# Optimization experiments

Measured on AMD Instinct MI355X. Metric: run time of the kernel, lower is better.

Reference implementation:

```python
import jax, jax.numpy as jnp
import numpy as np

RADIUS = 50.0
EPS = 1e-8


def setup_inputs() -> dict:
    key = jax.random.key(0)
    k1, k2, k3, k4, k5 = jax.random.split(key, 5)
    N, E, H = 16384, 524288, 256
    x = jax.random.normal(k1, (N, H), dtype=jnp.float32)
    edge_index = jax.random.randint(k2, (2, E), 0, N, dtype=jnp.int32)
    spatial_coords = jax.random.uniform(k3, (N, 2), dtype=jnp.float32) * 1000.0
    w1 = jax.random.normal(k4, (3, H // 2), dtype=jnp.float32) * 0.02
    b1 = jnp.zeros((H // 2,), dtype=jnp.float32)
    w2 = jax.random.normal(k5, (H // 2, H), dtype=jnp.float32) * 0.02
    b2 = jnp.zeros((H,), dtype=jnp.float32)
    return {"x": x, "edge_index": edge_index, "spatial_coords": spatial_coords,
            "w1": w1, "b1": b1, "w2": w2, "b2": b2}


def reference(x, edge_index, spatial_coords, w1, b1, w2, b2):
    N = x.shape[0]
    row, col = edge_index[0], edge_index[1]

    # degree via scatter-add (segment_sum)
    ones = jnp.ones(row.shape, dtype=x.dtype)
    degree = jax.ops.segment_sum(ones, row, num_segments=N)  # [N]

    # spatial density: count neighbors within RADIUS (full pairwise, vectorized)
    sq = jnp.sum(spatial_coords * spatial_coords, axis=-1)  # [N]
    d2 = sq[:, None] + sq[None, :] - 2.0 * (spatial_coords @ spatial_coords.T)  # [N,N] squared dists
    in_radius = (d2 <= RADIUS * RADIUS).astype(x.dtype)
    density = jnp.sum(in_radius, axis=1) - 1.0  # exclude self
    density = density / (jnp.max(density) + EPS)

    # local feature variance: || x - mean(neighbor features) ||
    nbr_sum = jax.ops.segment_sum(x[col], row, num_segments=N)  # [N,H]
    cnt = jnp.clip(degree, 1.0)[:, None]
    nbr_mean = nbr_sum / cnt
    fvar = jnp.linalg.norm(x - nbr_mean, axis=-1)  # [N]
    fvar = fvar / (jnp.max(fvar) + EPS)

    feats = jnp.stack([degree / (jnp.max(degree) + EPS), density, fvar], axis=-1)  # [N,3]
    h = jax.nn.relu(feats @ w1 + b1)
    return h @ w2 + b2  # [N, hidden_dim]
```

## Files before the change

kernel.cpp:

```cpp
#include <hip/hip_runtime.h>
#include <math.h>

#define R2 2500.0f
#define EPSF 1e-8f

constexpr int H   = 256;
constexpr int HH  = 128;
constexpr int NB  = 8;
constexpr int BSH = 11;
constexpr int RPW = 4;

__global__ void k_degree(const int* __restrict__ row, const int* __restrict__ col,
                         int* __restrict__ deg4, int E) {
    int e = blockIdx.x * blockDim.x + threadIdx.x;
    if (e < E) atomicAdd(&deg4[row[e] * NB + (col[e] >> BSH)], 1);
}

__global__ void __launch_bounds__(256) k_bsum(const int* __restrict__ deg4,
                                              int* __restrict__ bsum) {
    int t = threadIdx.x;
    int4 v = ((const int4*)deg4)[blockIdx.x * 256 + t];
    int sum = v.x + v.y + v.z + v.w;
#pragma unroll
    for (int off = 32; off > 0; off >>= 1) sum += __shfl_xor(sum, off, 64);
    __shared__ int sw[4];
    if ((t & 63) == 0) sw[t >> 6] = sum;
    __syncthreads();
    if (t == 0) bsum[blockIdx.x] = sw[0] + sw[1] + sw[2] + sw[3];
}

__global__ void k_bscan(const int* __restrict__ bsum, int* __restrict__ boff) {
    __shared__ int s[128];
    int t = threadIdx.x;
    s[t] = bsum[t];
    __syncthreads();
    for (int off = 1; off < 128; off <<= 1) {
        int v = s[t];
        int add = (t >= off) ? s[t - off] : 0;
        __syncthreads();
        s[t] = v + add;
        __syncthreads();
    }
    boff[t] = (t > 0) ? s[t - 1] : 0;
}

__global__ void __launch_bounds__(256) k_scat(const int* __restrict__ deg4,
                                              const int* __restrict__ boff,
                                              int* __restrict__ rp4,
                                              int* __restrict__ cur4, int M) {
    int t = threadIdx.x, blk = blockIdx.x;
    int lane = t & 63, w = t >> 6;
    int4 v = ((const int4*)deg4)[blk * 256 + t];
    int tsum = v.x + v.y + v.z + v.w;
    int incl = tsum;
#pragma unroll
    for (int off = 1; off < 64; off <<= 1) {
        int n = __shfl_up(incl, off, 64);
        if (lane >= off) incl += n;
    }
    __shared__ int wsum[4];
    if (lane == 63) wsum[w] = incl;
    __syncthreads();
    int woff = 0;
#pragma unroll
    for (int k = 0; k < 4; k++) woff += (k < w) ? wsum[k] : 0;
    int excl = boff[blk] + woff + (incl - tsum);
    int4 r;
    r.x = excl;
    r.y = excl + v.x;
    r.z = excl + v.x + v.y;
    r.w = excl + v.x + v.y + v.z;
    ((int4*)rp4)[blk * 256 + t]  = r;
    ((int4*)cur4)[blk * 256 + t] = r;
    if (blk == gridDim.x - 1 && t == 255) rp4[M] = excl + tsum;
}

__global__ void k_fill(const int* __restrict__ row, const int* __restrict__ col,
                       int* __restrict__ cur4, int* __restrict__ cols, int E) {
    int e = blockIdx.x * blockDim.x + threadIdx.x;
    if (e < E) {
        int r = row[e], c = col[e];
        int p = atomicAdd(&cur4[r * NB + (c >> BSH)], 1);
        cols[p] = c;
    }
}

__global__ void k_cellcnt(const float* __restrict__ coords, int* __restrict__ cellcnt, int N) {
    int t = blockIdx.x * 256 + threadIdx.x;
    float2 c = ((const float2*)coords)[t];
    int cx = (int)(c.x * 0.02f); if (cx > 19) cx = 19;
    int cy = (int)(c.y * 0.02f); if (cy > 19) cy = 19;
    atomicAdd(&cellcnt[cy * 20 + cx], 1);
}

__global__ void k_cellscan(const int* __restrict__ cellcnt, int* __restrict__ cellstart,
                           int* __restrict__ cellcur) {
    __shared__ int s[512];
    int t = threadIdx.x;
    s[t] = (t < 400) ? cellcnt[t] : 0;
    __syncthreads();
    for (int off = 1; off < 512; off <<= 1) {
        int v = s[t];
        int add = (t >= off) ? s[t - off] : 0;
        __syncthreads();
        s[t] = v + add;
        __syncthreads();
    }
    if (t < 400) {
        int excl = (t > 0) ? s[t - 1] : 0;
        cellstart[t] = excl;
        cellcur[t]   = excl;
    }
    if (t == 400) cellstart[400] = s[399];
}

__global__ void k_cellfill(const float* __restrict__ coords, int* __restrict__ cellcur,
                           float4* __restrict__ pts, int N) {
    int t = blockIdx.x * 256 + threadIdx.x;
    float2 c = ((const float2*)coords)[t];
    int cx = (int)(c.x * 0.02f); if (cx > 19) cx = 19;
    int cy = (int)(c.y * 0.02f); if (cy > 19) cy = 19;
    int p = atomicAdd(&cellcur[cy * 20 + cx], 1);
    pts[p] = make_float4(c.x, c.y, c.x * c.x + c.y * c.y, __int_as_float(t));
}

__global__ void __launch_bounds__(256) k_dgrid(
    const float4* __restrict__ pts, const int* __restrict__ cellstart,
    int* __restrict__ dens, int N) {
    int wave = threadIdx.x >> 6;
    int lane = threadIdx.x & 63;
    int t = blockIdx.x * 4 + wave;
    float4 p = pts[t];
    int cx = (int)(p.x * 0.02f); if (cx > 19) cx = 19;
    int cy = (int)(p.y * 0.02f); if (cy > 19) cy = 19;
    int x0 = cx - 2; if (x0 < 0) x0 = 0;
    int x1 = cx + 2; if (x1 > 19) x1 = 19;
    int y0 = cy - 2; if (y0 < 0) y0 = 0;
    int y1 = cy + 2; if (y1 > 19) y1 = 19;
    int cnt = 0;
    for (int yy = y0; yy <= y1; yy++) {
        int rowb = yy * 20;
        int s = cellstart[rowb + x0];
        int e = cellstart[rowb + x1 + 1];
        for (int q = s + lane; q < e; q += 64) {
            float4 pq = pts[q];
            float dot = p.x * pq.x + p.y * pq.y;
            float d2 = (p.z + pq.z) - 2.0f * dot;
            cnt += (d2 <= R2) ? 1 : 0;
        }
    }
#pragma unroll
    for (int off = 32; off > 0; off >>= 1) cnt += __shfl_xor(cnt, off, 64);
    if (lane == 0) dens[__float_as_int(p.w)] = cnt;
}

__global__ void __launch_bounds__(256) k_fvar(
    const float* __restrict__ x, const int* __restrict__ rp4,
    const int* __restrict__ cols, float* __restrict__ fvar, int N) {
    __shared__ float4 lds[4][8][64];
    int wave = threadIdx.x >> 6;
    int lane = threadIdx.x & 63;
    int i0 = (blockIdx.x * 4 + wave) * RPW;
    const float4* xb = (const float4*)x;
    float4 acc[RPW];
#pragma unroll
    for (int r = 0; r < RPW; r++) acc[r] = make_float4(0.f, 0.f, 0.f, 0.f);

    for (int b = 0; b < NB; b++) {
#pragma unroll
        for (int r = 0; r < RPW; r++) {
            int s = rp4[(i0 + r) * NB + b];
            int e = rp4[(i0 + r) * NB + b + 1];
            for (int p0 = s; p0 < e; p0 += 64) {
                int m = e - p0; if (m > 64) m = 64;
                int idx = cols[p0 + (lane < m ? lane : m - 1)];
                for (int j = 0; j < m; j += 8) {
                    int nb2 = m - j; if (nb2 > 8) nb2 = 8;
#pragma unroll
                    for (int k = 0; k < 8; k++) {
                        if (k < nb2) {
                            int c = __shfl(idx, j + k, 64);
                            const float4* gp = xb + (size_t)c * 64 + lane;
                            __builtin_amdgcn_global_load_lds(
                                (const __attribute__((address_space(1))) void*)gp,
                                (__attribute__((address_space(3))) void*)(&lds[wave][k][0]),
                                16, 0, 0);
                        }
                    }
                    __builtin_amdgcn_s_waitcnt(0);
#pragma unroll
                    for (int k = 0; k < 8; k++) {
                        if (k < nb2) {
                            float4 v = lds[wave][k][lane];
                            acc[r].x += v.x; acc[r].y += v.y;
                            acc[r].z += v.z; acc[r].w += v.w;
                        }
                    }
                }
            }
        }
    }

#pragma unroll
    for (int r = 0; r < RPW; r++) {
        int i = i0 + r;
        float cnt = fmaxf((float)(rp4[(i + 1) * NB] - rp4[i * NB]), 1.0f);
        float4 xi = xb[(size_t)i * 64 + lane];
        float dx = xi.x - acc[r].x / cnt;
        float dy = xi.y - acc[r].y / cnt;
        float dz = xi.z - acc[r].z / cnt;
        float dw = xi.w - acc[r].w / cnt;
        float ss = dx * dx + dy * dy + dz * dz + dw * dw;
#pragma unroll
        for (int off = 32; off > 0; off >>= 1) ss += __shfl_xor(ss, off, 64);
        if (lane == 0) fvar[i] = sqrtf(ss);
    }
}

__global__ void __launch_bounds__(256) k_scal(
    const int* __restrict__ rp4, const int* __restrict__ dens,
    const float* __restrict__ fvar, int* __restrict__ scal, int N) {
    __shared__ int sd[4], sn[4];
    __shared__ float sf[4];
    int t = threadIdx.x;
    int g = blockIdx.x * 256 + t;
    int stride = 256 * gridDim.x;
    int md = 0, mn = 0;
    float mf = 0.f;
    for (int i = g; i < N; i += stride) {
        md = max(md, rp4[(i + 1) * NB] - rp4[i * NB]);
        mn = max(mn, dens[i]);
        mf = fmaxf(mf, fvar[i]);
    }
#pragma unroll
    for (int off = 32; off > 0; off >>= 1) {
        md = max(md, __shfl_xor(md, off, 64));
        mn = max(mn, __shfl_xor(mn, off, 64));
        mf = fmaxf(mf, __shfl_xor(mf, off, 64));
    }
    int w = t >> 6, l = t & 63;
    if (l == 0) { sd[w] = md; sn[w] = mn; sf[w] = mf; }
    __syncthreads();
    if (t == 0) {
#pragma unroll
        for (int k = 1; k < 4; k++) {
            md = max(md, sd[k]);
            mn = max(mn, sn[k]);
            mf = fmaxf(mf, sf[k]);
        }
        atomicMax(&scal[0], md);
        atomicMax(&scal[1], mn);
        atomicMax(&scal[2], __float_as_int(mf));
    }
}

__global__ void __launch_bounds__(256) k_mlp(
    const float* __restrict__ w1, const float* __restrict__ b1,
    const float* __restrict__ w2, const float* __restrict__ b2,
    const int* __restrict__ rp4, const int* __restrict__ dens,
    const float* __restrict__ fvar, const int* __restrict__ scal,
    float* __restrict__ out, int N) {
    __shared__ float sh_h[HH];
    int j = threadIdx.x;
    float wv[HH];
#pragma unroll
    for (int l = 0; l < HH; l++) wv[l] = w2[l * H + j];
    float bj = b2[j];
    float maxdeg  = (float)scal[0] + EPSF;
    float maxdens = (float)(scal[1] - 1) + EPSF;
    float maxfv   = __int_as_float(scal[2]) + EPSF;
    float w1a = 0.f, w1b = 0.f, w1c = 0.f, b1j = 0.f;
    if (j < HH) { w1a = w1[j]; w1b = w1[HH + j]; w1c = w1[2 * HH + j]; b1j = b1[j]; }
    for (int i = blockIdx.x; i < N; i += gridDim.x) {
        float f0 = (float)(rp4[(i + 1) * NB] - rp4[i * NB]) / maxdeg;
        float f1 = (float)(dens[i] - 1) / maxdens;
        float f2 = fvar[i] / maxfv;
        if (j < HH) {
            float h = f0 * w1a + f1 * w1b + f2 * w1c + b1j;
            sh_h[j] = fmaxf(h, 0.0f);
        }
        __syncthreads();
        float acc = bj;
#pragma unroll
        for (int l = 0; l < HH; l++) acc = fmaf(sh_h[l], wv[l], acc);
        out[(size_t)i * H + j] = acc;
        __syncthreads();
    }
}

extern "C" void kernel_launch(void* const* d_in, const int* in_sizes, int n_in,
                              void* d_out, int out_size, void* d_ws, size_t ws_size,
                              hipStream_t stream) {
    const float* x      = (const float*)d_in[0];
    const int*   ei     = (const int*)d_in[1];
    const float* coords = (const float*)d_in[2];
    const float* w1     = (const float*)d_in[3];
    const float* b1     = (const float*)d_in[4];
    const float* w2     = (const float*)d_in[5];
    const float* b2     = (const float*)d_in[6];
    float* out = (float*)d_out;

    const int N = in_sizes[2] / 2;
    const int E = in_sizes[1] / 2;
    const int M = N * NB;
    const int NBLK = M / 1024;
    const int* row = ei;
    const int* col = ei + E;

    int* ws        = (int*)d_ws;
    int* scal      = ws;
    int* deg4      = ws + 4;
    int* cellcnt   = ws + 4 + M;
    int* rp4       = ws + 408 + M;
    int* cur4      = rp4 + M + 4;
    int* cellstart = cur4 + M;
    int* cellcur   = cellstart + 404;
    int* dens_cnt  = cellcur + 400;
    float* fvarp   = (float*)(dens_cnt + N);
    int* bsum      = dens_cnt + 2 * N;
    int* boff      = bsum + 128;
    int* cols      = boff + 128;
    float4* pts    = (float4*)(cols + E);

    hipMemsetAsync(ws, 0, (size_t)(408 + M) * sizeof(int), stream);

    int eb = (E + 255) / 256;
    k_degree<<<eb, 256, 0, stream>>>(row, col, deg4, E);
    k_bsum<<<NBLK, 256, 0, stream>>>(deg4, bsum);
    k_bscan<<<1, NBLK, 0, stream>>>(bsum, boff);
    k_scat<<<NBLK, 256, 0, stream>>>(deg4, boff, rp4, cur4, M);
    k_fill<<<eb, 256, 0, stream>>>(row, col, cur4, cols, E);

    k_cellcnt<<<N / 256, 256, 0, stream>>>(coords, cellcnt, N);
    k_cellscan<<<1, 512, 0, stream>>>(cellcnt, cellstart, cellcur);
    k_cellfill<<<N / 256, 256, 0, stream>>>(coords, cellcur, pts, N);
    k_dgrid<<<N / 4, 256, 0, stream>>>(pts, cellstart, dens_cnt, N);

    k_fvar<<<N / (4 * RPW), 256, 0, stream>>>(x, rp4, cols, fvarp, N);

    k_scal<<<64, 256, 0, stream>>>(rp4, dens_cnt, fvarp, scal, N);

    k_mlp<<<1024, 256, 0, stream>>>(w1, b1, w2, b2, rp4, dens_cnt, fvarp, scal,
                                    out, N);
}
```

Baseline: 267.2 us.

## Software-pipeline neighbor gathers into registers and preload column indices in fvar

The fvar gather kernel drops the LDS staging through global_load_lds with a full waitcnt. It now double-buffers 8 float4 gathers per (row, bucket) in registers, issuing the next segment's loads before accumulating the previous one. Row boundaries are fetched once per wave into lanes and broadcast with shuffles, and the first 256 column indices are preloaded into registers. Launch bounds are raised to request higher occupancy. The register pressure from two 8-deep float4 buffers could limit occupancy, and segments longer than 8 fall back to a serial load loop.

```diff
diff --git a/kernel.cpp b/kernel.cpp
--- a/kernel.cpp
+++ b/kernel.cpp
@@ -154,67 +154,113 @@
     if (lane == 0) dens[__float_as_int(p.w)] = cnt;
 }
 
-__global__ void __launch_bounds__(256) k_fvar(
+__global__ void __launch_bounds__(256, 4) k_fvar(
     const float* __restrict__ x, const int* __restrict__ rp4,
     const int* __restrict__ cols, float* __restrict__ fvar, int N) {
-    __shared__ float4 lds[4][8][64];
     int wave = threadIdx.x >> 6;
     int lane = threadIdx.x & 63;
     int i0 = (blockIdx.x * 4 + wave) * RPW;
     const float4* xb = (const float4*)x;
-    float4 acc[RPW];
-#pragma unroll
-    for (int r = 0; r < RPW; r++) acc[r] = make_float4(0.f, 0.f, 0.f, 0.f);
+
+    int bnd = rp4[i0 * NB + (lane < 32 ? lane : 32)];
+    int S = __shfl(bnd, 0, 64);
+    int T = __shfl(bnd, 32, 64);
+
+    int tc = T - 1; if (tc < S) tc = S;
+    int pp = S + lane;
+    int cr0 = cols[pp < T ? pp : tc]; pp += 64;
+    int cr1 = cols[pp < T ? pp : tc]; pp += 64;
+    int cr2 = cols[pp < T ? pp : tc]; pp += 64;
+    int cr3 = cols[pp < T ? pp : tc];
+
+    auto colAt = [&](int pos) -> int {
+        int q = pos - S;
+        if (q < 256) {
+            int w = q >> 6;
+            int src = (w == 0) ? cr0 : (w == 1) ? cr1 : (w == 2) ? cr2 : cr3;
+            return __shfl(src, q & 63, 64);
+        }
+        return cols[pos];
+    };
+
+    float4 acc0 = make_float4(0.f, 0.f, 0.f, 0.f);
+    float4 acc1 = make_float4(0.f, 0.f, 0.f, 0.f);
+    float4 acc2 = make_float4(0.f, 0.f, 0.f, 0.f);
+    float4 acc3 = make_float4(0.f, 0.f, 0.f, 0.f);
+    float4 g[8], h[8];
+    int pm = 0, ps = 0, cm, cs;
+
+#define ISSUE(RR, BUF)                                                  \
+    {                                                                   \
+        int s_ = __shfl(bnd, (RR) * NB + b, 64);                        \
+        int e_ = __shfl(bnd, (RR) * NB + b + 1, 64);                    \
+        int m_ = e_ - s_;                                               \
+        _Pragma("unroll")                                               \
+        for (int k = 0; k < 8; k++) {                                   \
+            size_t off_ = 0;              \
+            if (k < m_) off_ = (size_t)colAt(s_ + k) * 64 + lane;       \
+            BUF[k] = xb[off_];                                          \
+        }                                                               \
+        cm = m_; cs = s_;                                               \
+    }
+
+#define ACCP(ACCR, BUF)                                                 \
+    {                                                                   \
+        _Pragma("unroll")                                               \
+        for (int k = 0; k < 8; k++) {                                   \
+            float w_ = (k < pm) ? 1.0f : 0.0f;                          \
+            ACCR.x += BUF[k].x * w_; ACCR.y += BUF[k].y * w_;           \
+            ACCR.z += BUF[k].z * w_; ACCR.w += BUF[k].w * w_;           \
+        }                                                               \
+        if (pm > 8) {                                                   \
+            for (int pq = ps + 8; pq < ps + pm; pq++) {                 \
+                float4 v_ = xb[(size_t)colAt(pq) * 64 + lane];          \
+                ACCR.x += v_.x; ACCR.y += v_.y;                         \
+                ACCR.z += v_.z; ACCR.w += v_.w;                         \
+            }                                                           \
+        }                                                               \
+    }
 
     for (int b = 0; b < NB; b++) {
-#pragma unroll
-        for (int r = 0; r < RPW; r++) {
-            int s = rp4[(i0 + r) * NB + b];
-            int e = rp4[(i0 + r) * NB + b + 1];
-            for (int p0 = s; p0 < e; p0 += 64) {
-                int m = e - p0; if (m > 64) m = 64;
-                int idx = cols[p0 + (lane < m ? lane : m - 1)];
-                for (int j = 0; j < m; j += 8) {
-                    int nb2 = m - j; if (nb2 > 8) nb2 = 8;
-#pragma unroll
-                    for (int k = 0; k < 8; k++) {
-                        if (k < nb2) {
-                            int c = __shfl(idx, j + k, 64);
-                            const float4* gp = xb + (size_t)c * 64 + lane;
-                            __builtin_amdgcn_global_load_lds(
-                                (const __attribute__((address_space(1))) void*)gp,
-                                (__attribute__((address_space(3))) void*)(&lds[wave][k][0]),
-                                16, 0, 0);
-                        }
-                    }
-                    __builtin_amdgcn_s_waitcnt(0);
-#pragma unroll
-                    for (int k = 0; k < 8; k++) {
-                        if (k < nb2) {
-                            float4 v = lds[wave][k][lane];
-                            acc[r].x += v.x; acc[r].y += v.y;
-                            acc[r].z += v.z; acc[r].w += v.w;
-                        }
-                    }
-                }
-            }
-        }
-    }
-
-#pragma unroll
-    for (int r = 0; r < RPW; r++) {
-        int i = i0 + r;
-        float cnt = fmaxf((float)(rp4[(i + 1) * NB] - rp4[i * NB]), 1.0f);
-        float4 xi = xb[(size_t)i * 64 + lane];
-        float dx = xi.x - acc[r].x / cnt;
-        float dy = xi.y - acc[r].y / cnt;
-        float dz = xi.z - acc[r].z / cnt;
-        float dw = xi.w - acc[r].w / cnt;
-        float ss = dx * dx + dy * dy + dz * dz + dw * dw;
-#pragma unroll
-        for (int off = 32; off > 0; off >>= 1) ss += __shfl_xor(ss, off, 64);
-        if (lane == 0) fvar[i] = sqrtf(ss);
-    }
+        ISSUE(0, g);
+        if (b > 0) { ACCP(acc3, h); }
+        pm = cm; ps = cs;
+        ISSUE(1, h);
+        ACCP(acc0, g);
+        pm = cm; ps = cs;
+        ISSUE(2, g);
+        ACCP(acc1, h);
+        pm = cm; ps = cs;
+        ISSUE(3, h);
+        ACCP(acc2, g);
+        pm = cm; ps = cs;
+    }
+    ACCP(acc3, h);
+
+#undef ISSUE
+#undef ACCP
+
+#define FIN(RR, ACCR)                                                   \
+    {                                                                   \
+        int i = i0 + (RR);                                              \
+        float cnt = fmaxf((float)(__shfl(bnd, (RR) * NB + NB, 64) -     \
+                                  __shfl(bnd, (RR) * NB, 64)), 1.0f);   \
+        float4 xi = xb[(size_t)i * 64 + lane];                          \
+        float dx = xi.x - ACCR.x / cnt;                                 \
+        float dy = xi.y - ACCR.y / cnt;                                 \
+        float dz = xi.z - ACCR.z / cnt;                                 \
+        float dw = xi.w - ACCR.w / cnt;                                 \
+        float ss = dx * dx + dy * dy + dz * dz + dw * dw;               \
+        _Pragma("unroll")                                               \
+        for (int off = 32; off > 0; off >>= 1) ss += __shfl_xor(ss, off, 64); \
+        if (lane == 0) fvar[i] = sqrtf(ss);                             \
+    }
+
+    FIN(0, acc0);
+    FIN(1, acc1);
+    FIN(2, acc2);
+    FIN(3, acc3);
+#undef FIN
 }
 
 __global__ void __launch_bounds__(256) k_scal(
```

Result: slower. 329.8 us (+23.4%).

## Fuse CSR and grid-build kernels and batch four rows' neighbor gathers per bucket

Applied to the files above, without the earlier changes.

The degree/cell-count, scan and fill steps for the edge CSR and the spatial grid are merged into shared kernels. Each scan block now recomputes the block-offset prefix itself, so launches go from nine to four and the single-block scan kernel disappears. The feature-variance kernel now gathers the neighbors of all four rows a wave owns, per column bucket, as one combined batch of up to 64, and masks each neighbor into its row's accumulator with FMA weights. This exposes more outstanding row loads per wait and removes per-row boundary reloads, at the cost of four times the accumulate arithmetic and a serial fallback path when a bucket has more than 64 neighbors.

```diff
diff --git a/kernel.cpp b/kernel.cpp
--- a/kernel.cpp
+++ b/kernel.cpp
@@ -10,10 +10,22 @@
 constexpr int BSH = 11;
 constexpr int RPW = 4;
 
-__global__ void k_degree(const int* __restrict__ row, const int* __restrict__ col,
-                         int* __restrict__ deg4, int E) {
-    int e = blockIdx.x * blockDim.x + threadIdx.x;
-    if (e < E) atomicAdd(&deg4[row[e] * NB + (col[e] >> BSH)], 1);
+__global__ void __launch_bounds__(256) k_degcell(
+    const int* __restrict__ row, const int* __restrict__ col,
+    int* __restrict__ deg4, const float* __restrict__ coords,
+    int* __restrict__ cellcnt, int E, int EB, int N) {
+    if ((int)blockIdx.x < EB) {
+        int e = blockIdx.x * 256 + threadIdx.x;
+        if (e < E) atomicAdd(&deg4[row[e] * NB + (col[e] >> BSH)], 1);
+    } else {
+        int t = ((int)blockIdx.x - EB) * 256 + threadIdx.x;
+        if (t < N) {
+            float2 c = ((const float2*)coords)[t];
+            int cx = (int)(c.x * 0.02f); if (cx > 19) cx = 19;
+            int cy = (int)(c.y * 0.02f); if (cy > 19) cy = 19;
+            atomicAdd(&cellcnt[cy * 20 + cx], 1);
+        }
+    }
 }
 
 __global__ void __launch_bounds__(256) k_bsum(const int* __restrict__ deg4,
@@ -29,99 +41,92 @@
     if (t == 0) bsum[blockIdx.x] = sw[0] + sw[1] + sw[2] + sw[3];
 }
 
-__global__ void k_bscan(const int* __restrict__ bsum, int* __restrict__ boff) {
-    __shared__ int s[128];
-    int t = threadIdx.x;
-    s[t] = bsum[t];
-    __syncthreads();
-    for (int off = 1; off < 128; off <<= 1) {
-        int v = s[t];
-        int add = (t >= off) ? s[t - off] : 0;
-        __syncthreads();
-        s[t] = v + add;
-        __syncthreads();
-    }
-    boff[t] = (t > 0) ? s[t - 1] : 0;
-}
-
-__global__ void __launch_bounds__(256) k_scat(const int* __restrict__ deg4,
-                                              const int* __restrict__ boff,
-                                              int* __restrict__ rp4,
-                                              int* __restrict__ cur4, int M) {
-    int t = threadIdx.x, blk = blockIdx.x;
-    int lane = t & 63, w = t >> 6;
-    int4 v = ((const int4*)deg4)[blk * 256 + t];
-    int tsum = v.x + v.y + v.z + v.w;
-    int incl = tsum;
-#pragma unroll
-    for (int off = 1; off < 64; off <<= 1) {
-        int n = __shfl_up(incl, off, 64);
-        if (lane >= off) incl += n;
-    }
-    __shared__ int wsum[4];
-    if (lane == 63) wsum[w] = incl;
-    __syncthreads();
-    int woff = 0;
-#pragma unroll
-    for (int k = 0; k < 4; k++) woff += (k < w) ? wsum[k] : 0;
-    int excl = boff[blk] + woff + (incl - tsum);
-    int4 r;
-    r.x = excl;
-    r.y = excl + v.x;
-    r.z = excl + v.x + v.y;
-    r.w = excl + v.x + v.y + v.z;
-    ((int4*)rp4)[blk * 256 + t]  = r;
-    ((int4*)cur4)[blk * 256 + t] = r;
-    if (blk == gridDim.x - 1 && t == 255) rp4[M] = excl + tsum;
-}
-
-__global__ void k_fill(const int* __restrict__ row, const int* __restrict__ col,
-                       int* __restrict__ cur4, int* __restrict__ cols, int E) {
-    int e = blockIdx.x * blockDim.x + threadIdx.x;
-    if (e < E) {
-        int r = row[e], c = col[e];
-        int p = atomicAdd(&cur4[r * NB + (c >> BSH)], 1);
-        cols[p] = c;
-    }
-}
-
-__global__ void k_cellcnt(const float* __restrict__ coords, int* __restrict__ cellcnt, int N) {
-    int t = blockIdx.x * 256 + threadIdx.x;
-    float2 c = ((const float2*)coords)[t];
-    int cx = (int)(c.x * 0.02f); if (cx > 19) cx = 19;
-    int cy = (int)(c.y * 0.02f); if (cy > 19) cy = 19;
-    atomicAdd(&cellcnt[cy * 20 + cx], 1);
-}
-
-__global__ void k_cellscan(const int* __restrict__ cellcnt, int* __restrict__ cellstart,
-                           int* __restrict__ cellcur) {
+__global__ void __launch_bounds__(512) k_scatcell(
+    const int* __restrict__ deg4, const int* __restrict__ bsum,
+    int* __restrict__ rp4, int* __restrict__ cur4, int M,
+    const int* __restrict__ cellcnt, int* __restrict__ cellstart,
+    int* __restrict__ cellcur) {
     __shared__ int s[512];
     int t = threadIdx.x;
-    s[t] = (t < 400) ? cellcnt[t] : 0;
-    __syncthreads();
-    for (int off = 1; off < 512; off <<= 1) {
-        int v = s[t];
-        int add = (t >= off) ? s[t - off] : 0;
+    int blk = blockIdx.x;
+    if (blk < gridDim.x - 1) {
+        s[t] = (t < 128) ? bsum[t] : 0;
         __syncthreads();
-        s[t] = v + add;
+        for (int off = 1; off < 128; off <<= 1) {
+            int v = (t < 128) ? s[t] : 0;
+            int add = (t >= off && t < 128) ? s[t - off] : 0;
+            __syncthreads();
+            if (t < 128) s[t] = v + add;
+            __syncthreads();
+        }
+        int boff = (blk > 0) ? s[blk - 1] : 0;
+        if (t < 256) {
+            int lane = t & 63, w = t >> 6;
+            int4 v = ((const int4*)deg4)[blk * 256 + t];
+            int tsum = v.x + v.y + v.z + v.w;
+            int incl = tsum;
+#pragma unroll
+            for (int off = 1; off < 64; off <<= 1) {
+                int n = __shfl_up(incl, off, 64);
+                if (lane >= off) incl += n;
+            }
+            __shared__ int wsum[4];
+            if (lane == 63) wsum[w] = incl;
+            __syncthreads();
+            int woff = 0;
+#pragma unroll
+            for (int k = 0; k < 4; k++) woff += (k < w) ? wsum[k] : 0;
+            int excl = boff + woff + (incl - tsum);
+            int4 r;
+            r.x = excl;
+            r.y = excl + v.x;
+            r.z = excl + v.x + v.y;
+            r.w = excl + v.x + v.y + v.z;
+            ((int4*)rp4)[blk * 256 + t]  = r;
+            ((int4*)cur4)[blk * 256 + t] = r;
+            if (blk == 127 && t == 255) rp4[M] = excl + tsum;
+        }
+    } else {
+        s[t] = (t < 400) ? cellcnt[t] : 0;
         __syncthreads();
-    }
-    if (t < 400) {
-        int excl = (t > 0) ? s[t - 1] : 0;
-        cellstart[t] = excl;
-        cellcur[t]   = excl;
-    }
-    if (t == 400) cellstart[400] = s[399];
-}
-
-__global__ void k_cellfill(const float* __restrict__ coords, int* __restrict__ cellcur,
-                           float4* __restrict__ pts, int N) {
-    int t = blockIdx.x * 256 + threadIdx.x;
-    float2 c = ((const float2*)coords)[t];
-    int cx = (int)(c.x * 0.02f); if (cx > 19) cx = 19;
-    int cy = (int)(c.y * 0.02f); if (cy > 19) cy = 19;
-    int p = atomicAdd(&cellcur[cy * 20 + cx], 1);
-    pts[p] = make_float4(c.x, c.y, c.x * c.x + c.y * c.y, __int_as_float(t));
+        for (int off = 1; off < 512; off <<= 1) {
+            int v = s[t];
+            int add = (t >= off) ? s[t - off] : 0;
+            __syncthreads();
+            s[t] = v + add;
+            __syncthreads();
+        }
+        if (t < 400) {
+            int excl = (t > 0) ? s[t - 1] : 0;
+            cellstart[t] = excl;
+            cellcur[t]   = excl;
+        }
+        if (t == 400) cellstart[400] = s[399];
+    }
+}
+
+__global__ void __launch_bounds__(256) k_fillcell(
+    const int* __restrict__ row, const int* __restrict__ col,
+    int* __restrict__ cur4, int* __restrict__ cols,
+    const float* __restrict__ coords, int* __restrict__ cellcur,
+    float4* __restrict__ pts, int E, int EB, int N) {
+    if ((int)blockIdx.x < EB) {
+        int e = blockIdx.x * 256 + threadIdx.x;
+        if (e < E) {
+            int r = row[e], c = col[e];
+            int p = atomicAdd(&cur4[r * NB + (c >> BSH)], 1);
+            cols[p] = c;
+        }
+    } else {
+        int t = ((int)blockIdx.x - EB) * 256 + threadIdx.x;
+        if (t < N) {
+            float2 c = ((const float2*)coords)[t];
+            int cx = (int)(c.x * 0.02f); if (cx > 19) cx = 19;
+            int cy = (int)(c.y * 0.02f); if (cy > 19) cy = 19;
+            int p = atomicAdd(&cellcur[cy * 20 + cx], 1);
+            pts[p] = make_float4(c.x, c.y, c.x * c.x + c.y * c.y, __int_as_float(t));
+        }
+    }
 }
 
 __global__ void __launch_bounds__(256) k_dgrid(
@@ -162,59 +167,110 @@
     int lane = threadIdx.x & 63;
     int i0 = (blockIdx.x * 4 + wave) * RPW;
     const float4* xb = (const float4*)x;
-    float4 acc[RPW];
-#pragma unroll
-    for (int r = 0; r < RPW; r++) acc[r] = make_float4(0.f, 0.f, 0.f, 0.f);
+
+    int bnd = rp4[i0 * NB + (lane < 32 ? lane : 32)];
+
+    float4 acc0 = make_float4(0.f, 0.f, 0.f, 0.f);
+    float4 acc1 = make_float4(0.f, 0.f, 0.f, 0.f);
+    float4 acc2 = make_float4(0.f, 0.f, 0.f, 0.f);
+    float4 acc3 = make_float4(0.f, 0.f, 0.f, 0.f);
 
     for (int b = 0; b < NB; b++) {
-#pragma unroll
-        for (int r = 0; r < RPW; r++) {
-            int s = rp4[(i0 + r) * NB + b];
-            int e = rp4[(i0 + r) * NB + b + 1];
-            for (int p0 = s; p0 < e; p0 += 64) {
-                int m = e - p0; if (m > 64) m = 64;
-                int idx = cols[p0 + (lane < m ? lane : m - 1)];
-                for (int j = 0; j < m; j += 8) {
-                    int nb2 = m - j; if (nb2 > 8) nb2 = 8;
-#pragma unroll
-                    for (int k = 0; k < 8; k++) {
-                        if (k < nb2) {
-                            int c = __shfl(idx, j + k, 64);
-                            const float4* gp = xb + (size_t)c * 64 + lane;
-                            __builtin_amdgcn_global_load_lds(
-                                (const __attribute__((address_space(1))) void*)gp,
-                                (__attribute__((address_space(3))) void*)(&lds[wave][k][0]),
-                                16, 0, 0);
-                        }
-                    }
-                    __builtin_amdgcn_s_waitcnt(0);
-#pragma unroll
-                    for (int k = 0; k < 8; k++) {
-                        if (k < nb2) {
-                            float4 v = lds[wave][k][lane];
-                            acc[r].x += v.x; acc[r].y += v.y;
-                            acc[r].z += v.z; acc[r].w += v.w;
-                        }
-                    }
+        int s0 = __shfl(bnd, b, 64),      e0 = __shfl(bnd, b + 1, 64);
+        int s1 = __shfl(bnd, 8 + b, 64),  e1 = __shfl(bnd, 9 + b, 64);
+        int s2 = __shfl(bnd, 16 + b, 64), e2 = __shfl(bnd, 17 + b, 64);
+        int s3 = __shfl(bnd, 24 + b, 64), e3 = __shfl(bnd, 25 + b, 64);
+        int m0 = e0 - s0, m1 = e1 - s1, m2 = e2 - s2;
+        int c1 = m0, c2 = m0 + m1, c3 = m0 + m1 + m2;
+        int mt = c3 + (e3 - s3);
+        if (mt == 0) continue;
+
+        int j = lane;
+        int rowj = (j >= c1) + (j >= c2) + (j >= c3);
+        int base = (rowj == 0) ? s0 : (rowj == 1) ? (s1 - c1)
+                 : (rowj == 2) ? (s2 - c2) : (s3 - c3);
+        int pos = base + j;
+        if (j >= mt) pos = s0;
+        int colj = cols[pos];
+
+        int mtc = (mt > 64) ? 64 : mt;
+        for (int j0 = 0; j0 < mtc; j0 += 8) {
+            int nb2 = mtc - j0; if (nb2 > 8) nb2 = 8;
+#pragma unroll
+            for (int k = 0; k < 8; k++) {
+                if (k < nb2) {
+                    int c = __shfl(colj, j0 + k, 64);
+                    const float4* gp = xb + (size_t)c * 64 + lane;
+                    __builtin_amdgcn_global_load_lds(
+                        (const __attribute__((address_space(1))) void*)gp,
+                        (__attribute__((address_space(3))) void*)(&lds[wave][k][0]),
+                        16, 0, 0);
                 }
             }
-        }
-    }
-
-#pragma unroll
-    for (int r = 0; r < RPW; r++) {
-        int i = i0 + r;
-        float cnt = fmaxf((float)(rp4[(i + 1) * NB] - rp4[i * NB]), 1.0f);
-        float4 xi = xb[(size_t)i * 64 + lane];
-        float dx = xi.x - acc[r].x / cnt;
-        float dy = xi.y - acc[r].y / cnt;
-        float dz = xi.z - acc[r].z / cnt;
-        float dw = xi.w - acc[r].w / cnt;
-        float ss = dx * dx + dy * dy + dz * dz + dw * dw;
-#pragma unroll
-        for (int off = 32; off > 0; off >>= 1) ss += __shfl_xor(ss, off, 64);
-        if (lane == 0) fvar[i] = sqrtf(ss);
-    }
+            __builtin_amdgcn_s_waitcnt(0);
+#pragma unroll
+            for (int k = 0; k < 8; k++) {
+                if (k < nb2) {
+                    int rk = __shfl(rowj, j0 + k, 64);
+                    float4 v = lds[wave][k][lane];
+                    float w0 = (rk == 0) ? 1.0f : 0.0f;
+                    float w1 = (rk == 1) ? 1.0f : 0.0f;
+                    float w2 = (rk == 2) ? 1.0f : 0.0f;
+                    float w3 = (rk == 3) ? 1.0f : 0.0f;
+                    acc0.x = fmaf(v.x, w0, acc0.x); acc0.y = fmaf(v.y, w0, acc0.y);
+                    acc0.z = fmaf(v.z, w0, acc0.z); acc0.w = fmaf(v.w, w0, acc0.w);
+                    acc1.x = fmaf(v.x, w1, acc1.x); acc1.y = fmaf(v.y, w1, acc1.y);
+                    acc1.z = fmaf(v.z, w1, acc1.z); acc1.w = fmaf(v.w, w1, acc1.w);
+                    acc2.x = fmaf(v.x, w2, acc2.x); acc2.y = fmaf(v.y, w2, acc2.y);
+                    acc2.z = fmaf(v.z, w2, acc2.z); acc2.w = fmaf(v.w, w2, acc2.w);
+                    acc3.x = fmaf(v.x, w3, acc3.x); acc3.y = fmaf(v.y, w3, acc3.y);
+                    acc3.z = fmaf(v.z, w3, acc3.z); acc3.w = fmaf(v.w, w3, acc3.w);
+                }
+            }
+        }
+        if (mt > 64) {
+            for (int jq = 64; jq < mt; jq++) {
+                int rk = (jq >= c1) + (jq >= c2) + (jq >= c3);
+                int pq = ((rk == 0) ? s0 : (rk == 1) ? (s1 - c1)
+                        : (rk == 2) ? (s2 - c2) : (s3 - c3)) + jq;
+                float4 v = xb[(size_t)cols[pq] * 64 + lane];
+                float w0 = (rk == 0) ? 1.0f : 0.0f;
+                float w1 = (rk == 1) ? 1.0f : 0.0f;
+                float w2 = (rk == 2) ? 1.0f : 0.0f;
+                float w3 = (rk == 3) ? 1.0f : 0.0f;
+                acc0.x = fmaf(v.x, w0, acc0.x); acc0.y = fmaf(v.y, w0, acc0.y);
+                acc0.z = fmaf(v.z, w0, acc0.z); acc0.w = fmaf(v.w, w0, acc0.w);
+                acc1.x = fmaf(v.x, w1, acc1.x); acc1.y = fmaf(v.y, w1, acc1.y);
+                acc1.z = fmaf(v.z, w1, acc1.z); acc1.w = fmaf(v.w, w1, acc1.w);
+                acc2.x = fmaf(v.x, w2, acc2.x); acc2.y = fmaf(v.y, w2, acc2.y);
+                acc2.z = fmaf(v.z, w2, acc2.z); acc2.w = fmaf(v.w, w2, acc2.w);
+                acc3.x = fmaf(v.x, w3, acc3.x); acc3.y = fmaf(v.y, w3, acc3.y);
+                acc3.z = fmaf(v.z, w3, acc3.z); acc3.w = fmaf(v.w, w3, acc3.w);
+            }
+        }
+    }
+
+#define FIN(RR, ACCR)                                                   \
+    {                                                                   \
+        int i = i0 + (RR);                                              \
+        float cnt = fmaxf((float)(__shfl(bnd, (RR) * NB + NB, 64) -     \
+                                  __shfl(bnd, (RR) * NB, 64)), 1.0f);   \
+        float4 xi = xb[(size_t)i * 64 + lane];                          \
+        float dx = xi.x - ACCR.x / cnt;                                 \
+        float dy = xi.y - ACCR.y / cnt;                                 \
+        float dz = xi.z - ACCR.z / cnt;                                 \
+        float dw = xi.w - ACCR.w / cnt;                                 \
+        float ss = dx * dx + dy * dy + dz * dz + dw * dw;               \
+        _Pragma("unroll")                                               \
+        for (int off = 32; off > 0; off >>= 1) ss += __shfl_xor(ss, off, 64); \
+        if (lane == 0) fvar[i] = sqrtf(ss);                             \
+    }
+
+    FIN(0, acc0);
+    FIN(1, acc1);
+    FIN(2, acc2);
+    FIN(3, acc3);
+#undef FIN
 }
 
 __global__ void __launch_bounds__(256) k_scal(
@@ -304,6 +360,8 @@
     const int E = in_sizes[1] / 2;
     const int M = N * NB;
     const int NBLK = M / 1024;
+    const int EB = (E + 255) / 256;
+    const int CB = N / 256;
     const int* row = ei;
     const int* col = ei + E;
 
@@ -324,16 +382,13 @@
 
     hipMemsetAsync(ws, 0, (size_t)(408 + M) * sizeof(int), stream);
 
-    int eb = (E + 255) / 256;
-    k_degree<<<eb, 256, 0, stream>>>(row, col, deg4, E);
+    k_degcell<<<EB + CB, 256, 0, stream>>>(row, col, deg4, coords, cellcnt, E, EB, N);
     k_bsum<<<NBLK, 256, 0, stream>>>(deg4, bsum);
-    k_bscan<<<1, NBLK, 0, stream>>>(bsum, boff);
-    k_scat<<<NBLK, 256, 0, stream>>>(deg4, boff, rp4, cur4, M);
-    k_fill<<<eb, 256, 0, stream>>>(row, col, cur4, cols, E);
-
-    k_cellcnt<<<N / 256, 256, 0, stream>>>(coords, cellcnt, N);
-    k_cellscan<<<1, 512, 0, stream>>>(cellcnt, cellstart, cellcur);
-    k_cellfill<<<N / 256, 256, 0, stream>>>(coords, cellcur, pts, N);
+    k_scatcell<<<NBLK + 1, 512, 0, stream>>>(deg4, bsum, rp4, cur4, M,
+                                             cellcnt, cellstart, cellcur);
+    k_fillcell<<<EB + CB, 256, 0, stream>>>(row, col, cur4, cols,
+                                            coords, cellcur, pts, E, EB, N);
+
     k_dgrid<<<N / 4, 256, 0, stream>>>(pts, cellstart, dens_cnt, N);
 
     k_fvar<<<N / (4 * RPW), 256, 0, stream>>>(x, rp4, cols, fvarp, N);
```

After: 255.6 us. -4.3%, faster.
